# Optimization experiments

Hardware: AMD Instinct MI355X
Metric: run time of the kernel (lower is better)

The kernel has to match this reference:

```python
import jax, jax.numpy as jnp
import numpy as np

L, P, D, NH, RBF, NL = 256, 1024, 256, 4, 50, 2
HD = D // NH
EPS = 1e-5


def _layernorm(x, g, b):
    mu = x.mean(-1, keepdims=True)
    var = ((x - mu) ** 2).mean(-1, keepdims=True)
    return (x - mu) * jax.lax.rsqrt(var + EPS) * g + b


def setup_inputs() -> dict:
    key = jax.random.key(0)
    ks = iter(jax.random.split(key, 64))
    def nrm(shape, s=0.02):
        return jax.random.normal(next(ks), shape, dtype=jnp.float32) * s
    inp = {
        "protein_features": jax.random.normal(next(ks), (1, P, 20), jnp.float32),
        "ligand_features": jax.random.normal(next(ks), (1, L, 20), jnp.float32),
        "protein_positions": jax.random.normal(next(ks), (1, P, 3), jnp.float32),
        "ligand_positions": jax.random.normal(next(ks), (1, L, 3), jnp.float32),
        "pair_rbf": jax.random.uniform(next(ks), (1, L, P, RBF), jnp.float32),
        # encoders
        "pe_w1": nrm((20, D)), "pe_b1": jnp.zeros((D,)),
        "pe_w2": nrm((D, D)), "pe_b2": jnp.zeros((D,)),
        "le_w1": nrm((20, D)), "le_b1": jnp.zeros((D,)),
        "le_w2": nrm((D, D)), "le_b2": jnp.zeros((D,)),
        # cross-attn layers stacked over NL
        "qw": nrm((NL, D, D)), "qb": jnp.zeros((NL, D)),
        "kw": nrm((NL, D, D)), "kb": jnp.zeros((NL, D)),
        "vw": nrm((NL, D, D)), "vb": jnp.zeros((NL, D)),
        "rw": nrm((NL, RBF, NH)), "rb": jnp.zeros((NL, NH)),
        "ow": nrm((NL, D, D)), "ob": jnp.zeros((NL, D)),
        "ln_g": jnp.ones((NL, D)), "ln_b": jnp.zeros((NL, D)),
        # gated pooling
        "pg_w1": nrm((D, D // 2)), "pg_b1": jnp.zeros((D // 2,)),
        "pg_w2": nrm((D // 2, 1)), "pg_b2": jnp.zeros((1,)),
        # heads
        "af_w1": nrm((D, D)), "af_b1": jnp.zeros((D,)),
        "af_w2": nrm((D, 1)), "af_b2": jnp.zeros((1,)),
        "cf_w1": nrm((D, D // 2)), "cf_b1": jnp.zeros((D // 2,)),
        "cf_w2": nrm((D // 2, 1)), "cf_b2": jnp.zeros((1,)),
        "iw1": nrm((2 * D + RBF, D)), "ib1": jnp.zeros((D,)),
        "iw2": nrm((D, 5)), "ib2": jnp.zeros((5,)),
    }
    return inp


def reference(protein_features, ligand_features, protein_positions, ligand_positions,
              pair_rbf, pe_w1, pe_b1, pe_w2, pe_b2, le_w1, le_b1, le_w2, le_b2,
              qw, qb, kw, kb, vw, vb, rw, rb, ow, ob, ln_g, ln_b,
              pg_w1, pg_b1, pg_w2, pg_b2, af_w1, af_b1, af_w2, af_b2,
              cf_w1, cf_b1, cf_w2, cf_b2, iw1, ib1, iw2, ib2):
    pf = protein_features[0]          # [P, 20]
    lf = ligand_features[0]           # [L, 20]
    rbf = pair_rbf[0]                 # [L, P, RBF]

    prot_h = jax.nn.silu(pf @ pe_w1 + pe_b1) @ pe_w2 + pe_b2   # [P, D]
    lig_h = jax.nn.silu(lf @ le_w1 + le_b1) @ le_w2 + le_b2    # [L, D]

    scale = float(HD) ** 0.5
    attn_w = None
    for i in range(NL):
        Q = (lig_h @ qw[i] + qb[i]).reshape(L, NH, HD)
        K = (prot_h @ kw[i] + kb[i]).reshape(P, NH, HD)
        V = (prot_h @ vw[i] + vb[i]).reshape(P, NH, HD)
        scores = jnp.einsum('lhd,phd->lph', Q, K) / scale      # [L, P, NH]
        scores = scores + (rbf @ rw[i] + rb[i])                # RBF additive bias per head
        attn_w = jax.nn.softmax(scores, axis=1)                # softmax over protein axis
        attended = jnp.einsum('lph,phd->lhd', attn_w, V).reshape(L, D)
        lig_h = _layernorm(lig_h + attended @ ow[i] + ob[i], ln_g[i], ln_b[i])

    gate_logits = jnp.tanh(lig_h @ pg_w1 + pg_b1) @ pg_w2 + pg_b2  # [L, 1]
    gate = jax.nn.softmax(gate_logits, axis=0)
    complex_repr = (gate * lig_h).sum(axis=0, keepdims=True)        # [1, D]

    pkd = jax.nn.silu(complex_repr @ af_w1 + af_b1) @ af_w2 + af_b2
    conf = jax.nn.sigmoid(jax.nn.silu(complex_repr @ cf_w1 + cf_b1) @ cf_w2 + cf_b2)
    docking_score = pkd * conf

    lig_exp = jnp.broadcast_to(lig_h[:, None, :], (L, P, D))
    prot_exp = jnp.broadcast_to(prot_h[None, :, :], (L, P, D))
    pair_input = jnp.concatenate([lig_exp, prot_exp, rbf], axis=-1)  # [L, P, 2D+RBF]
    imap = jax.nn.sigmoid(jax.nn.silu(pair_input @ iw1 + ib1) @ iw2 + ib2)

    attn_out = attn_w.mean(axis=-1).reshape(1, L * P)
    return (docking_score, pkd, conf, imap[None], attn_out)
```

## Files before the change

### kernel.cpp

```cpp
#include <hip/hip_runtime.h>
#include <math.h>

#define LN_ 256
#define PN_ 1024
#define DN_ 256
#define NH_ 4
#define RBF_N 50
#define NL_ 2
#define HD_ 64
#define EPSV 1e-5f
#define LP_ (LN_ * PN_)

typedef __attribute__((ext_vector_type(8))) short bf16x8;
typedef __attribute__((ext_vector_type(4))) float f32x4;

__device__ __forceinline__ float fast_sigmoid(float x){ return 1.f/(1.f+__expf(-x)); }
__device__ __forceinline__ float fast_silu(float x){ return x/(1.f+__expf(-x)); }
__device__ __forceinline__ short f2bf(float x){
  union { float f; unsigned u; } v; v.f = x;
  unsigned r = v.u + 0x7FFF + ((v.u >> 16) & 1);
  return (short)(r >> 16);
}

struct GSeg {
  const float* A; const float* W; const float* bias; float* C;
  int K; int act; int transOut;
};
struct GArgs { GSeg s[3]; int b0, b1; };

__global__ __launch_bounds__(256) void gemm8(GArgs ga)
{
  extern __shared__ float sA[];
  int bid = blockIdx.x;
  int si = (bid < ga.b0) ? 0 : (bid < ga.b1 ? 1 : 2);
  int base = (si == 0) ? 0 : ((si == 1) ? ga.b0 : ga.b1);
  GSeg sg = ga.s[si];
  int row0 = (bid - base) * 8;
  int K = sg.K;
  int t = threadIdx.x;
  for (int idx = t; idx < 8 * K; idx += 256) {
    int r = idx / K, k = idx - r * K;
    sA[idx] = sg.A[(size_t)(row0 + r) * K + k];
  }
  __syncthreads();
  float acc[8];
  float bv = sg.bias ? sg.bias[t] : 0.f;
  #pragma unroll
  for (int r = 0; r < 8; r++) acc[r] = bv;
  for (int k = 0; k < K; k++) {
    float w = sg.W[(size_t)k * DN_ + t];
    #pragma unroll
    for (int r = 0; r < 8; r++) acc[r] = fmaf(sA[r * K + k], w, acc[r]);
  }
  #pragma unroll
  for (int r = 0; r < 8; r++) {
    float v = acc[r];
    if (sg.act == 1) v = fast_silu(v);
    if (sg.transOut) sg.C[(size_t)t * PN_ + row0 + r] = v;
    else             sg.C[(size_t)(row0 + r) * DN_ + t] = v;
  }
}

__global__ __launch_bounds__(256) void rbf_transpose(
    const float* __restrict__ rbf, float* __restrict__ rbfT)
{
  __shared__ float ld[256][RBF_N + 1];
  int t = threadIdx.x;
  size_t base = (size_t)blockIdx.x << 8;
  const float* src = rbf + base * RBF_N;
  for (int i = 0; i < RBF_N; i++) {
    int fl = i * 256 + t;
    int row = fl / RBF_N, colk = fl - row * RBF_N;
    ld[row][colk] = src[fl];
  }
  __syncthreads();
  for (int k = 0; k < RBF_N; k++)
    rbfT[(size_t)k * LP_ + base + t] = ld[t][k];
}

__global__ __launch_bounds__(256) void wr_pack(
    const float* __restrict__ Wr, short* __restrict__ WT)
{
  int d = threadIdx.x;
  for (int k = 0; k < 64; k++)
    WT[d * 64 + k] = (k < RBF_N) ? f2bf(Wr[k * DN_ + d]) : (short)0;
}

__global__ __launch_bounds__(256) void scores_softmax_l(
    const float* __restrict__ Q, const float* __restrict__ Kt,
    const float* __restrict__ rbfT, const float* __restrict__ rw,
    const float* __restrict__ rb, float* __restrict__ attn,
    float* __restrict__ amean)
{
  int l = blockIdx.x, t = threadIdx.x, lane = t & 63, wv = t >> 6;
  __shared__ float qs[DN_];
  __shared__ float rws[NH_][RBF_N];
  __shared__ float redm[16], reds[16];
  qs[t] = Q[(size_t)l * DN_ + t];
  if (t < RBF_N * NH_) rws[t & 3][t >> 2] = rw[t];
  __syncthreads();

  float sc[NH_][4];
  for (int i = 0; i < 4; i++) {
    int p = t + (i << 8);
    size_t idx = ((size_t)l << 10) + p;
    float s2[NH_] = {0.f, 0.f, 0.f, 0.f};
    #pragma unroll 10
    for (int k = 0; k < RBF_N; k++) {
      float rv = rbfT[(size_t)k * LP_ + idx];
      s2[0] = fmaf(rv, rws[0][k], s2[0]);
      s2[1] = fmaf(rv, rws[1][k], s2[1]);
      s2[2] = fmaf(rv, rws[2][k], s2[2]);
      s2[3] = fmaf(rv, rws[3][k], s2[3]);
    }
    #pragma unroll
    for (int h = 0; h < NH_; h++) {
      const float* kp = Kt + ((size_t)(h << 6) << 10) + p;
      float a = 0.f;
      #pragma unroll 8
      for (int d = 0; d < HD_; d++) a = fmaf(qs[(h << 6) + d], kp[(size_t)d << 10], a);
      sc[h][i] = a * 0.125f + s2[h] + rb[h];
    }
  }

  float mh[NH_];
  #pragma unroll
  for (int h = 0; h < NH_; h++) {
    float m = fmaxf(fmaxf(sc[h][0], sc[h][1]), fmaxf(sc[h][2], sc[h][3]));
    for (int o = 32; o > 0; o >>= 1) m = fmaxf(m, __shfl_xor(m, o));
    if (lane == 0) redm[h * 4 + wv] = m;
  }
  __syncthreads();
  #pragma unroll
  for (int h = 0; h < NH_; h++)
    mh[h] = fmaxf(fmaxf(redm[h * 4 + 0], redm[h * 4 + 1]),
                  fmaxf(redm[h * 4 + 2], redm[h * 4 + 3]));

  float e[NH_][4], inv[NH_];
  #pragma unroll
  for (int h = 0; h < NH_; h++) {
    float s = 0.f;
    #pragma unroll
    for (int i = 0; i < 4; i++) { e[h][i] = __expf(sc[h][i] - mh[h]); s += e[h][i]; }
    for (int o = 32; o > 0; o >>= 1) s += __shfl_xor(s, o);
    if (lane == 0) reds[h * 4 + wv] = s;
  }
  __syncthreads();
  #pragma unroll
  for (int h = 0; h < NH_; h++)
    inv[h] = 1.f / (reds[h * 4 + 0] + reds[h * 4 + 1] + reds[h * 4 + 2] + reds[h * 4 + 3]);

  #pragma unroll
  for (int h = 0; h < NH_; h++)
    for (int i = 0; i < 4; i++)
      attn[(((size_t)(l << 2) + h) << 10) + t + (i << 8)] = e[h][i] * inv[h];

  if (amean) {
    for (int i = 0; i < 4; i++) {
      float s = e[0][i] * inv[0] + e[1][i] * inv[1] + e[2][i] * inv[2] + e[3][i] * inv[3];
      amean[((size_t)l << 10) + t + (i << 8)] = s * 0.25f;
    }
  }
}

__global__ __launch_bounds__(256) void attend_proj_ln(
    const float* __restrict__ attn, const float* __restrict__ V,
    const float* __restrict__ ow, const float* __restrict__ ob,
    const float* __restrict__ g, const float* __restrict__ bb,
    float* __restrict__ lig)
{
  int l = blockIdx.x, t = threadIdx.x, lane = t & 63, wv = t >> 6;
  int h = t >> 6, d = t & 63;
  __shared__ float as[DN_];
  __shared__ float red[8];
  const float* aw = attn + (((size_t)(l << 2) + h) << 10);
  const float* Vp = V + (h << 6) + d;
  float acc = 0.f;
  #pragma unroll 8
  for (int p = 0; p < PN_; p++) acc = fmaf(aw[p], Vp[(size_t)p << 8], acc);
  as[t] = acc;
  __syncthreads();
  float acc2 = ob[t];
  #pragma unroll 4
  for (int k = 0; k < DN_; k++) acc2 = fmaf(as[k], ow[(size_t)(k << 8) + t], acc2);
  float x = lig[((size_t)l << 8) + t] + acc2;
  float sm = x;
  for (int o = 32; o > 0; o >>= 1) sm += __shfl_xor(sm, o);
  if (lane == 0) red[wv] = sm;
  __syncthreads();
  float mu = (red[0] + red[1] + red[2] + red[3]) * (1.f / DN_);
  float dx = x - mu;
  float v = dx * dx;
  for (int o = 32; o > 0; o >>= 1) v += __shfl_xor(v, o);
  if (lane == 0) red[4 + wv] = v;
  __syncthreads();
  float var = (red[4] + red[5] + red[6] + red[7]) * (1.f / DN_);
  lig[((size_t)l << 8) + t] = dx * (1.f / sqrtf(var + EPSV)) * g[t] + bb[t];
}

__global__ __launch_bounds__(128) void gate_logits_k(
    const float* __restrict__ lig, const float* __restrict__ w1,
    const float* __restrict__ b1, const float* __restrict__ w2,
    const float* __restrict__ b2, float* __restrict__ glog)
{
  int l = blockIdx.x, n = threadIdx.x, lane = n & 63, wv = n >> 6;
  __shared__ float ls[DN_];
  __shared__ float red[2];
  ls[n] = lig[(size_t)l * DN_ + n];
  ls[n + 128] = lig[(size_t)l * DN_ + n + 128];
  __syncthreads();
  float acc = b1[n];
  #pragma unroll 4
  for (int k = 0; k < DN_; k++) acc = fmaf(ls[k], w1[k * 128 + n], acc);
  float part = tanhf(acc) * w2[n];
  for (int o = 32; o > 0; o >>= 1) part += __shfl_xor(part, o);
  if (lane == 0) red[wv] = part;
  __syncthreads();
  if (n == 0) glog[l] = red[0] + red[1] + b2[0];
}

__global__ __launch_bounds__(256) void pool_heads(
    const float* __restrict__ lig, const float* __restrict__ glog,
    const float* __restrict__ afw1, const float* __restrict__ afb1,
    const float* __restrict__ afw2, const float* __restrict__ afb2,
    const float* __restrict__ cfw1, const float* __restrict__ cfb1,
    const float* __restrict__ cfw2, const float* __restrict__ cfb2,
    float* __restrict__ out)
{
  __shared__ float wsh[LN_];
  __shared__ float cr[DN_];
  __shared__ float h1s[DN_];
  __shared__ float h2s[128];
  __shared__ float red[8];
  int t = threadIdx.x, lane = t & 63, wv = t >> 6;
  float x = glog[t];
  float m = x;
  for (int o = 32; o > 0; o >>= 1) m = fmaxf(m, __shfl_xor(m, o));
  if (lane == 0) red[wv] = m;
  __syncthreads();
  m = fmaxf(fmaxf(red[0], red[1]), fmaxf(red[2], red[3]));
  float e = __expf(x - m);
  float s = e;
  for (int o = 32; o > 0; o >>= 1) s += __shfl_xor(s, o);
  if (lane == 0) red[4 + wv] = s;
  __syncthreads();
  s = red[4] + red[5] + red[6] + red[7];
  wsh[t] = e / s;
  __syncthreads();
  float acc = 0.f;
  #pragma unroll 4
  for (int l2 = 0; l2 < LN_; l2++) acc = fmaf(wsh[l2], lig[(size_t)l2 * DN_ + t], acc);
  cr[t] = acc;
  __syncthreads();
  float a = afb1[t];
  #pragma unroll 4
  for (int d = 0; d < DN_; d++) a = fmaf(cr[d], afw1[d * DN_ + t], a);
  h1s[t] = fast_silu(a);
  if (t < 128) {
    float c = cfb1[t];
    #pragma unroll 4
    for (int d = 0; d < DN_; d++) c = fmaf(cr[d], cfw1[d * 128 + t], c);
    h2s[t] = fast_silu(c);
  }
  __syncthreads();
  float pp = h1s[t] * afw2[t];
  for (int o = 32; o > 0; o >>= 1) pp += __shfl_xor(pp, o);
  if (lane == 0) red[wv] = pp;
  float cp = (t < 128) ? h2s[t] * cfw2[t] : 0.f;
  for (int o = 32; o > 0; o >>= 1) cp += __shfl_xor(cp, o);
  if (lane == 0) red[4 + wv] = cp;
  __syncthreads();
  if (t == 0) {
    float pkd = red[0] + red[1] + red[2] + red[3] + afb2[0];
    float cl  = red[4] + red[5] + red[6] + red[7] + cfb2[0];
    float conf = fast_sigmoid(cl);
    out[0] = pkd * conf;
    out[1] = pkd;
    out[2] = conf;
  }
}

#define RSTR 72
#define BTP2 133
union PairSMem {
  short R[128 * RSTR];
  float B[2][16 * BTP2];
};
__global__ __launch_bounds__(512, 6) void pair_main4(
    const float* __restrict__ A, const float* __restrict__ BT,
    const float* __restrict__ rbf, const short* __restrict__ WT,
    const float* __restrict__ w2, const float* __restrict__ ib2,
    float* __restrict__ imap)
{
  __shared__ PairSMem u;
  __shared__ float sw2[DN_ * 5];
  __shared__ float sAl[DN_];

  int t = threadIdx.x;
  int lane = t & 63, wid = t >> 6;
  int bid = blockIdx.x;
  int l = bid >> 3;
  int p0 = (bid & 7) << 7;

  {
    unsigned* rz = (unsigned*)u.R;
    #pragma unroll
    for (int i = 0; i < 9; i++) rz[t + i * 512] = 0u;
  }
  __syncthreads();
  {
    const float* src = rbf + ((size_t)(l << 10) + p0) * RBF_N;
    #pragma unroll
    for (int i = 0; i < 13; i++) {
      int idx = t + i * 512;
      if (idx < 128 * RBF_N) {
        int row = idx / RBF_N, k = idx - row * RBF_N;
        u.R[row * RSTR + k] = f2bf(src[idx]);
      }
    }
  }
  for (int i = t; i < DN_ * 5; i += 512) sw2[i] = w2[i];
  if (t < DN_) sAl[t] = A[((size_t)l << 8) + t];
  __syncthreads();

  int m = lane & 15, gq = lane >> 4;
  bf16x8 a0 = *(const bf16x8*)&u.R[(wid * 16 + m) * RSTR + 0 + gq * 8];
  bf16x8 a1 = *(const bf16x8*)&u.R[(wid * 16 + m) * RSTR + 32 + gq * 8];
  __syncthreads();

  int srow = t >> 7, scol = t & 127;
  #pragma unroll
  for (int i = 0; i < 4; i++)
    u.B[0][(srow + 4 * i) * BTP2 + scol] =
        BT[(size_t)(srow + 4 * i) * PN_ + p0 + scol];
  __syncthreads();

  float acc5[4][5];
  #pragma unroll
  for (int r = 0; r < 4; r++)
    #pragma unroll
    for (int o = 0; o < 5; o++) acc5[r][o] = 0.f;

  int cur = 0;
  for (int nt = 0; nt < 16; nt++) {
    float ld0 = 0.f, ld1 = 0.f, ld2 = 0.f, ld3 = 0.f;
    if (nt < 15) {
      const float* bsrc = BT + (size_t)((nt + 1) * 16 + srow) * PN_ + p0 + scol;
      ld0 = bsrc[0];
      ld1 = bsrc[(size_t)4 * PN_];
      ld2 = bsrc[(size_t)8 * PN_];
      ld3 = bsrc[(size_t)12 * PN_];
    }

    int n = nt * 16 + m;
    bf16x8 b0 = *(const bf16x8*)&WT[n * 64 + gq * 8];
    bf16x8 b1 = *(const bf16x8*)&WT[n * 64 + 32 + gq * 8];
    f32x4 acc = {0.f, 0.f, 0.f, 0.f};
    acc = __builtin_amdgcn_mfma_f32_16x16x32_bf16(a0, b0, acc, 0, 0, 0);
    acc = __builtin_amdgcn_mfma_f32_16x16x32_bf16(a1, b1, acc, 0, 0, 0);
    float bA = sAl[n];
    const float* bp = &u.B[cur][m * BTP2 + wid * 16 + gq * 4];
    #pragma unroll
    for (int r = 0; r < 4; r++) {
      float h = acc[r] + bA + bp[r];
      float sh = fast_silu(h);
      #pragma unroll
      for (int o = 0; o < 5; o++)
        acc5[r][o] = fmaf(sh, sw2[n * 5 + o], acc5[r][o]);
    }
    __syncthreads();
    if (nt < 15) {
      float* bd = &u.B[cur ^ 1][srow * BTP2 + scol];
      bd[0 * 4 * BTP2] = ld0;
      bd[1 * 4 * BTP2] = ld1;
      bd[2 * 4 * BTP2] = ld2;
      bd[3 * 4 * BTP2] = ld3;
      __syncthreads();
      cur ^= 1;
    }
  }

  #pragma unroll
  for (int r = 0; r < 4; r++)
    #pragma unroll
    for (int o = 0; o < 5; o++) {
      float v = acc5[r][o];
      v += __shfl_xor(v, 1);
      v += __shfl_xor(v, 2);
      v += __shfl_xor(v, 4);
      v += __shfl_xor(v, 8);
      acc5[r][o] = v;
    }

  if (m < 5) {
    float bo = ib2[m];
    #pragma unroll
    for (int r = 0; r < 4; r++) {
      float v = 0.f;
      #pragma unroll
      for (int o = 0; o < 5; o++) if (m == o) v = acc5[r][o];
      int p = p0 + wid * 16 + gq * 4 + r;
      imap[((size_t)(l << 10) + p) * 5 + m] = fast_sigmoid(v + bo);
    }
  }
}

extern "C" void kernel_launch(void* const* d_in, const int* in_sizes, int n_in,
                              void* d_out, int out_size, void* d_ws, size_t ws_size,
                              hipStream_t stream)
{
  const float* pf    = (const float*)d_in[0];
  const float* lf    = (const float*)d_in[1];
  const float* rbf   = (const float*)d_in[4];
  const float* pe_w1 = (const float*)d_in[5];
  const float* pe_b1 = (const float*)d_in[6];
  const float* pe_w2 = (const float*)d_in[7];
  const float* pe_b2 = (const float*)d_in[8];
  const float* le_w1 = (const float*)d_in[9];
  const float* le_b1 = (const float*)d_in[10];
  const float* le_w2 = (const float*)d_in[11];
  const float* le_b2 = (const float*)d_in[12];
  const float* qw = (const float*)d_in[13];
  const float* qb = (const float*)d_in[14];
  const float* kw = (const float*)d_in[15];
  const float* kb = (const float*)d_in[16];
  const float* vw = (const float*)d_in[17];
  const float* vb = (const float*)d_in[18];
  const float* rw = (const float*)d_in[19];
  const float* rb = (const float*)d_in[20];
  const float* ow = (const float*)d_in[21];
  const float* ob = (const float*)d_in[22];
  const float* ln_g = (const float*)d_in[23];
  const float* ln_b = (const float*)d_in[24];
  const float* pg_w1 = (const float*)d_in[25];
  const float* pg_b1 = (const float*)d_in[26];
  const float* pg_w2 = (const float*)d_in[27];
  const float* pg_b2 = (const float*)d_in[28];
  const float* af_w1 = (const float*)d_in[29];
  const float* af_b1 = (const float*)d_in[30];
  const float* af_w2 = (const float*)d_in[31];
  const float* af_b2 = (const float*)d_in[32];
  const float* cf_w1 = (const float*)d_in[33];
  const float* cf_b1 = (const float*)d_in[34];
  const float* cf_w2 = (const float*)d_in[35];
  const float* cf_b2 = (const float*)d_in[36];
  const float* iw1 = (const float*)d_in[37];
  const float* ib1 = (const float*)d_in[38];
  const float* iw2 = (const float*)d_in[39];
  const float* ib2 = (const float*)d_in[40];

  float* out = (float*)d_out;

  float* w = (float*)d_ws;
  size_t off = 0;
  float* prot_h = w + off; off += (size_t)PN_ * DN_;
  float* lig_h  = w + off; off += (size_t)LN_ * DN_;
  float* ph1    = w + off; off += (size_t)PN_ * DN_;
  float* lh1    = w + off; off += (size_t)LN_ * DN_;
  float* Qb     = w + off; off += (size_t)LN_ * DN_;
  float* Kt     = w + off; off += (size_t)DN_ * PN_;
  float* Vb     = w + off; off += (size_t)PN_ * DN_;
  float* attn   = w + off; off += (size_t)LN_ * NH_ * PN_;
  float* pairA  = w + off; off += (size_t)LN_ * DN_;
  float* glog   = w + off; off += LN_;
  off = (off + 255) & ~(size_t)255;
  float* WrBF   = w + off; off += (size_t)DN_ * 64 / 2;
  off = (off + 255) & ~(size_t)255;
  float* rbfT   = w + off; off += (size_t)RBF_N * LP_;

  const int PB = PN_ / 8;
  const int LB = LN_ / 8;
  const size_t smax = 8 * DN_ * sizeof(float);

  rbf_transpose<<<LP_ / 256, 256, 0, stream>>>(rbf, rbfT);
  wr_pack<<<1, 256, 0, stream>>>(iw1 + (size_t)2 * DN_ * DN_, (short*)WrBF);

  {
    GArgs ga;
    ga.s[0] = { pf, pe_w1, pe_b1, ph1, 20, 1, 0 };
    ga.s[1] = { lf, le_w1, le_b1, lh1, 20, 1, 0 };
    ga.s[2] = ga.s[1];
    ga.b0 = PB; ga.b1 = PB + LB;
    gemm8<<<PB + LB, 256, smax, stream>>>(ga);
  }
  {
    GArgs ga;
    ga.s[0] = { ph1, pe_w2, pe_b2, prot_h, DN_, 0, 0 };
    ga.s[1] = { lh1, le_w2, le_b2, lig_h, DN_, 0, 0 };
    ga.s[2] = ga.s[1];
    ga.b0 = PB; ga.b1 = PB + LB;
    gemm8<<<PB + LB, 256, smax, stream>>>(ga);
  }

  for (int i = 0; i < NL_; i++) {
    const size_t wo = (size_t)i * DN_ * DN_;
    {
      GArgs ga;
      ga.s[0] = { lig_h,  qw + wo, qb + i * DN_, Qb, DN_, 0, 0 };
      ga.s[1] = { prot_h, kw + wo, kb + i * DN_, Kt, DN_, 0, 1 };
      ga.s[2] = { prot_h, vw + wo, vb + i * DN_, Vb, DN_, 0, 0 };
      ga.b0 = LB; ga.b1 = LB + PB;
      gemm8<<<LB + 2 * PB, 256, smax, stream>>>(ga);
    }
    scores_softmax_l<<<LN_, 256, 0, stream>>>(
        Qb, Kt, rbfT, rw + (size_t)i * RBF_N * NH_, rb + i * NH_, attn,
        (i == NL_ - 1) ? (out + 3 + (size_t)LN_ * PN_ * 5) : nullptr);
    attend_proj_ln<<<LN_, 256, 0, stream>>>(attn, Vb, ow + wo, ob + i * DN_,
                                            ln_g + i * DN_, ln_b + i * DN_, lig_h);
  }

  gate_logits_k<<<LN_, 128, 0, stream>>>(lig_h, pg_w1, pg_b1, pg_w2, pg_b2, glog);
  pool_heads<<<1, 256, 0, stream>>>(lig_h, glog, af_w1, af_b1, af_w2, af_b2,
                                    cf_w1, cf_b1, cf_w2, cf_b2, out);

  {
    GArgs ga;
    ga.s[0] = { lig_h,  iw1,                       ib1,     pairA, DN_, 0, 0 };
    ga.s[1] = { prot_h, iw1 + (size_t)DN_ * DN_,   nullptr, Kt,    DN_, 0, 1 };
    ga.s[2] = ga.s[1];
    ga.b0 = LB; ga.b1 = LB + PB;
    gemm8<<<LB + PB, 256, smax, stream>>>(ga);
  }

  pair_main4<<<(LN_ * PN_) / 128, 512, 0, stream>>>(
      pairA, Kt, rbf, (const short*)WrBF, iw2, ib2, out + 3);
}
```

Baseline: 715.2 us.

## Precompute RBF head bias for both layers and fuse attention layer kernels

The RBF transpose kernel becomes one that computes the per-head RBF bias for both layers in a single pass over pair_rbf. Each layer's score computation then reads a compact 4-float bias per pair instead of rereading the 50-channel transposed RBF. Scores, softmax, attention-weighted V, output projection and layernorm are fused into one 512-thread kernel per ligand row that keeps attention weights in shared memory, removing the attn buffer round trip and one launch per layer. The cost is larger per-block shared memory use and only 256 blocks per layer.

```diff
diff --git a/kernel.cpp b/kernel.cpp
--- a/kernel.cpp
+++ b/kernel.cpp
@@ -61,10 +61,12 @@
   }
 }
 
-__global__ __launch_bounds__(256) void rbf_transpose(
-    const float* __restrict__ rbf, float* __restrict__ rbfT)
+__global__ __launch_bounds__(256) void rbf_bias(
+    const float* __restrict__ rbf, const float* __restrict__ rw,
+    float* __restrict__ sL0, float* __restrict__ sL1)
 {
   __shared__ float ld[256][RBF_N + 1];
+  __shared__ float rwsh[2 * RBF_N * NH_];
   int t = threadIdx.x;
   size_t base = (size_t)blockIdx.x << 8;
   const float* src = rbf + base * RBF_N;
@@ -73,9 +75,23 @@
     int row = fl / RBF_N, colk = fl - row * RBF_N;
     ld[row][colk] = src[fl];
   }
-  __syncthreads();
-  for (int k = 0; k < RBF_N; k++)
-    rbfT[(size_t)k * LP_ + base + t] = ld[t][k];
+  for (int i = t; i < 2 * RBF_N * NH_; i += 256) rwsh[i] = rw[i];
+  __syncthreads();
+  #pragma unroll
+  for (int layer = 0; layer < 2; layer++) {
+    f32x4 acc = {0.f, 0.f, 0.f, 0.f};
+    const float* rwl = rwsh + layer * RBF_N * NH_;
+    #pragma unroll 10
+    for (int k = 0; k < RBF_N; k++) {
+      float rv = ld[t][k];
+      acc[0] = fmaf(rv, rwl[k * 4 + 0], acc[0]);
+      acc[1] = fmaf(rv, rwl[k * 4 + 1], acc[1]);
+      acc[2] = fmaf(rv, rwl[k * 4 + 2], acc[2]);
+      acc[3] = fmaf(rv, rwl[k * 4 + 3], acc[3]);
+    }
+    float* dst = (layer == 0 ? sL0 : sL1) + (base + t) * 4;
+    *(f32x4*)dst = acc;
+  }
 }
 
 __global__ __launch_bounds__(256) void wr_pack(
@@ -86,116 +102,118 @@
     WT[d * 64 + k] = (k < RBF_N) ? f2bf(Wr[k * DN_ + d]) : (short)0;
 }
 
-__global__ __launch_bounds__(256) void scores_softmax_l(
+__global__ __launch_bounds__(512) void layer_fused(
     const float* __restrict__ Q, const float* __restrict__ Kt,
-    const float* __restrict__ rbfT, const float* __restrict__ rw,
-    const float* __restrict__ rb, float* __restrict__ attn,
+    const float* __restrict__ V, const float* __restrict__ s2,
+    const float* __restrict__ rbp, const float* __restrict__ ow,
+    const float* __restrict__ ob, const float* __restrict__ g,
+    const float* __restrict__ bb, float* __restrict__ lig,
     float* __restrict__ amean)
 {
+  __shared__ float qs[DN_];
+  __shared__ float asm_[NH_][PN_];
+  __shared__ float redm[NH_][8], reds[NH_][8];
+  __shared__ float part[2][256];
+  __shared__ float as_[DN_];
+  __shared__ float red[8];
+
   int l = blockIdx.x, t = threadIdx.x, lane = t & 63, wv = t >> 6;
-  __shared__ float qs[DN_];
-  __shared__ float rws[NH_][RBF_N];
-  __shared__ float redm[16], reds[16];
-  qs[t] = Q[(size_t)l * DN_ + t];
-  if (t < RBF_N * NH_) rws[t & 3][t >> 2] = rw[t];
-  __syncthreads();
-
-  float sc[NH_][4];
-  for (int i = 0; i < 4; i++) {
-    int p = t + (i << 8);
-    size_t idx = ((size_t)l << 10) + p;
-    float s2[NH_] = {0.f, 0.f, 0.f, 0.f};
-    #pragma unroll 10
-    for (int k = 0; k < RBF_N; k++) {
-      float rv = rbfT[(size_t)k * LP_ + idx];
-      s2[0] = fmaf(rv, rws[0][k], s2[0]);
-      s2[1] = fmaf(rv, rws[1][k], s2[1]);
-      s2[2] = fmaf(rv, rws[2][k], s2[2]);
-      s2[3] = fmaf(rv, rws[3][k], s2[3]);
-    }
+  if (t < DN_) qs[t] = Q[(size_t)l * DN_ + t];
+  __syncthreads();
+
+  float sc[NH_][2];
+  #pragma unroll
+  for (int i = 0; i < 2; i++) {
+    int p = t + (i << 9);
+    f32x4 s2v = *(const f32x4*)(s2 + ((size_t)(l << 10) + p) * 4);
     #pragma unroll
     for (int h = 0; h < NH_; h++) {
       const float* kp = Kt + ((size_t)(h << 6) << 10) + p;
       float a = 0.f;
       #pragma unroll 8
       for (int d = 0; d < HD_; d++) a = fmaf(qs[(h << 6) + d], kp[(size_t)d << 10], a);
-      sc[h][i] = a * 0.125f + s2[h] + rb[h];
-    }
-  }
-
+      sc[h][i] = a * 0.125f + s2v[h] + rbp[h];
+    }
+  }
+
+  #pragma unroll
+  for (int h = 0; h < NH_; h++) {
+    float m = fmaxf(sc[h][0], sc[h][1]);
+    for (int o = 32; o > 0; o >>= 1) m = fmaxf(m, __shfl_xor(m, o));
+    if (lane == 0) redm[h][wv] = m;
+  }
+  __syncthreads();
   float mh[NH_];
   #pragma unroll
   for (int h = 0; h < NH_; h++) {
-    float m = fmaxf(fmaxf(sc[h][0], sc[h][1]), fmaxf(sc[h][2], sc[h][3]));
-    for (int o = 32; o > 0; o >>= 1) m = fmaxf(m, __shfl_xor(m, o));
-    if (lane == 0) redm[h * 4 + wv] = m;
-  }
-  __syncthreads();
-  #pragma unroll
-  for (int h = 0; h < NH_; h++)
-    mh[h] = fmaxf(fmaxf(redm[h * 4 + 0], redm[h * 4 + 1]),
-                  fmaxf(redm[h * 4 + 2], redm[h * 4 + 3]));
-
-  float e[NH_][4], inv[NH_];
+    float m = redm[h][0];
+    #pragma unroll
+    for (int i = 1; i < 8; i++) m = fmaxf(m, redm[h][i]);
+    mh[h] = m;
+  }
+  float e[NH_][2];
   #pragma unroll
   for (int h = 0; h < NH_; h++) {
-    float s = 0.f;
-    #pragma unroll
-    for (int i = 0; i < 4; i++) { e[h][i] = __expf(sc[h][i] - mh[h]); s += e[h][i]; }
+    e[h][0] = __expf(sc[h][0] - mh[h]);
+    e[h][1] = __expf(sc[h][1] - mh[h]);
+    float s = e[h][0] + e[h][1];
     for (int o = 32; o > 0; o >>= 1) s += __shfl_xor(s, o);
-    if (lane == 0) reds[h * 4 + wv] = s;
-  }
-  __syncthreads();
-  #pragma unroll
-  for (int h = 0; h < NH_; h++)
-    inv[h] = 1.f / (reds[h * 4 + 0] + reds[h * 4 + 1] + reds[h * 4 + 2] + reds[h * 4 + 3]);
-
-  #pragma unroll
-  for (int h = 0; h < NH_; h++)
-    for (int i = 0; i < 4; i++)
-      attn[(((size_t)(l << 2) + h) << 10) + t + (i << 8)] = e[h][i] * inv[h];
-
+    if (lane == 0) reds[h][wv] = s;
+  }
+  __syncthreads();
+  float am0 = 0.f, am1 = 0.f;
+  #pragma unroll
+  for (int h = 0; h < NH_; h++) {
+    float s = reds[h][0];
+    #pragma unroll
+    for (int i = 1; i < 8; i++) s += reds[h][i];
+    float inv = 1.f / s;
+    float a0 = e[h][0] * inv, a1 = e[h][1] * inv;
+    asm_[h][t] = a0;
+    asm_[h][t + 512] = a1;
+    am0 += a0; am1 += a1;
+  }
   if (amean) {
-    for (int i = 0; i < 4; i++) {
-      float s = e[0][i] * inv[0] + e[1][i] * inv[1] + e[2][i] * inv[2] + e[3][i] * inv[3];
-      amean[((size_t)l << 10) + t + (i << 8)] = s * 0.25f;
-    }
-  }
-}
-
-__global__ __launch_bounds__(256) void attend_proj_ln(
-    const float* __restrict__ attn, const float* __restrict__ V,
-    const float* __restrict__ ow, const float* __restrict__ ob,
-    const float* __restrict__ g, const float* __restrict__ bb,
-    float* __restrict__ lig)
-{
-  int l = blockIdx.x, t = threadIdx.x, lane = t & 63, wv = t >> 6;
-  int h = t >> 6, d = t & 63;
-  __shared__ float as[DN_];
-  __shared__ float red[8];
-  const float* aw = attn + (((size_t)(l << 2) + h) << 10);
-  const float* Vp = V + (h << 6) + d;
-  float acc = 0.f;
-  #pragma unroll 8
-  for (int p = 0; p < PN_; p++) acc = fmaf(aw[p], Vp[(size_t)p << 8], acc);
-  as[t] = acc;
-  __syncthreads();
-  float acc2 = ob[t];
-  #pragma unroll 4
-  for (int k = 0; k < DN_; k++) acc2 = fmaf(as[k], ow[(size_t)(k << 8) + t], acc2);
-  float x = lig[((size_t)l << 8) + t] + acc2;
+    amean[((size_t)l << 10) + t] = am0 * 0.25f;
+    amean[((size_t)l << 10) + t + 512] = am1 * 0.25f;
+  }
+  __syncthreads();
+
+  {
+    int g2 = t >> 8, c = t & 255;
+    const float* ap = asm_[c >> 6];
+    float acc = 0.f;
+    int pbeg = g2 << 9;
+    #pragma unroll 8
+    for (int p = pbeg; p < pbeg + 512; p++)
+      acc = fmaf(ap[p], V[((size_t)p << 8) + c], acc);
+    part[g2][c] = acc;
+  }
+  __syncthreads();
+  if (t < 256) as_[t] = part[0][t] + part[1][t];
+  __syncthreads();
+
+  float x = 0.f;
+  if (t < 256) {
+    float acc2 = ob[t];
+    #pragma unroll 4
+    for (int k = 0; k < DN_; k++) acc2 = fmaf(as_[k], ow[(size_t)(k << 8) + t], acc2);
+    x = lig[((size_t)l << 8) + t] + acc2;
+  }
   float sm = x;
   for (int o = 32; o > 0; o >>= 1) sm += __shfl_xor(sm, o);
-  if (lane == 0) red[wv] = sm;
+  if (t < 256 && lane == 0) red[wv] = sm;
   __syncthreads();
   float mu = (red[0] + red[1] + red[2] + red[3]) * (1.f / DN_);
   float dx = x - mu;
   float v = dx * dx;
   for (int o = 32; o > 0; o >>= 1) v += __shfl_xor(v, o);
-  if (lane == 0) red[4 + wv] = v;
-  __syncthreads();
-  float var = (red[4] + red[5] + red[6] + red[7]) * (1.f / DN_);
-  lig[((size_t)l << 8) + t] = dx * (1.f / sqrtf(var + EPSV)) * g[t] + bb[t];
+  if (t < 256 && lane == 0) red[4 + wv] = v;
+  __syncthreads();
+  if (t < 256) {
+    float var = (red[4] + red[5] + red[6] + red[7]) * (1.f / DN_);
+    lig[((size_t)l << 8) + t] = dx * (1.f / sqrtf(var + EPSV)) * g[t] + bb[t];
+  }
 }
 
 __global__ __launch_bounds__(128) void gate_logits_k(
@@ -351,7 +369,6 @@
       ld2 = bsrc[(size_t)8 * PN_];
       ld3 = bsrc[(size_t)12 * PN_];
     }
-
     int n = nt * 16 + m;
     bf16x8 b0 = *(const bf16x8*)&WT[n * 64 + gq * 8];
     bf16x8 b1 = *(const bf16x8*)&WT[n * 64 + 32 + gq * 8];
@@ -460,19 +477,19 @@
   float* Qb     = w + off; off += (size_t)LN_ * DN_;
   float* Kt     = w + off; off += (size_t)DN_ * PN_;
   float* Vb     = w + off; off += (size_t)PN_ * DN_;
-  float* attn   = w + off; off += (size_t)LN_ * NH_ * PN_;
   float* pairA  = w + off; off += (size_t)LN_ * DN_;
   float* glog   = w + off; off += LN_;
   off = (off + 255) & ~(size_t)255;
   float* WrBF   = w + off; off += (size_t)DN_ * 64 / 2;
   off = (off + 255) & ~(size_t)255;
-  float* rbfT   = w + off; off += (size_t)RBF_N * LP_;
+  float* sL0    = w + off; off += (size_t)LP_ * NH_;
+  float* sL1    = w + off; off += (size_t)LP_ * NH_;
 
   const int PB = PN_ / 8;
   const int LB = LN_ / 8;
   const size_t smax = 8 * DN_ * sizeof(float);
 
-  rbf_transpose<<<LP_ / 256, 256, 0, stream>>>(rbf, rbfT);
+  rbf_bias<<<LP_ / 256, 256, 0, stream>>>(rbf, rw, sL0, sL1);
   wr_pack<<<1, 256, 0, stream>>>(iw1 + (size_t)2 * DN_ * DN_, (short*)WrBF);
 
   {
@@ -502,11 +519,10 @@
       ga.b0 = LB; ga.b1 = LB + PB;
       gemm8<<<LB + 2 * PB, 256, smax, stream>>>(ga);
     }
-    scores_softmax_l<<<LN_, 256, 0, stream>>>(
-        Qb, Kt, rbfT, rw + (size_t)i * RBF_N * NH_, rb + i * NH_, attn,
+    layer_fused<<<LN_, 512, 0, stream>>>(
+        Qb, Kt, Vb, (i == 0) ? sL0 : sL1, rb + i * NH_,
+        ow + wo, ob + i * DN_, ln_g + i * DN_, ln_b + i * DN_, lig_h,
         (i == NL_ - 1) ? (out + 3 + (size_t)LN_ * PN_ * 5) : nullptr);
-    attend_proj_ln<<<LN_, 256, 0, stream>>>(attn, Vb, ow + wo, ob + i * DN_,
-                                            ln_g + i * DN_, ln_b + i * DN_, lig_h);
   }
 
   gate_logits_k<<<LN_, 128, 0, stream>>>(lig_h, pg_w1, pg_b1, pg_w2, pg_b2, glog);
```

New measurement: 598.1 us. -16.4%, faster.
